# Optimization experiments

Hardware: AMD Instinct MI355X
Metric: run time of the kernel (lower is better)

Reference implementation:

```python
import jax, jax.numpy as jnp
import numpy as np

B, N, F_DIM, C_DIM, L = 4, 2048, 64, 64, 3

def setup_inputs() -> dict:
    key = jax.random.key(0)
    k1, k2, k3 = jax.random.split(key, 3)
    V = jax.random.normal(k1, (B, N, F_DIM), dtype=jnp.float32)
    A = jax.random.uniform(k2, (B, N, N, L), dtype=jnp.float32)
    h_weights = jax.random.normal(k3, (L + 1, C_DIM, F_DIM), dtype=jnp.float32) * 0.05
    return {"V": V, "A": A, "h_weights": h_weights}

def reference(V, A, h_weights):
    # Original math: A_aug = concat([I, A], -1)  (identity as edge-type 0)
    # H[b,i,j,c,f] = sum_l A_aug[b,i,j,l] * h_weights[l,c,f]
    # V_out[b,i,c] = sum_{j,f} H[b,i,j,c,f] * V[b,j,f]; relu.
    # The identity edge-type contributes h_weights[0] @ V[b,i] directly,
    # avoiding materializing the concatenated (B,N,N,L+1) tensor.
    self_term = jnp.einsum('cf,bif->bic', h_weights[0], V)        # (B,N,C)
    rel_term = jnp.einsum('bijl,lcf,bjf->bic', A, h_weights[1:], V)
    return jax.nn.relu(self_term + rel_term)
```

## Files before the change

kernel.cpp:

```cpp
#include <hip/hip_runtime.h>
#include <cstdint>

#define BDIM 4
#define NDIM 2048
#define FDIM 64
#define CDIM 64
#define LDIM 3
#define KTOT (NDIM * LDIM)
#define BK 256
#define NSTEP (KTOT / BK)
#define KB (KTOT / 32)

typedef __attribute__((ext_vector_type(4))) float f32x4;
typedef __attribute__((ext_vector_type(8))) short s16x8;
typedef __attribute__((ext_vector_type(4))) unsigned int u32x4;

__device__ __forceinline__ unsigned short f2bf(float x) {
  union { float f; uint32_t u; } v; v.f = x;
  uint32_t r = v.u + 0x7FFFu + ((v.u >> 16) & 1u);
  return (unsigned short)(r >> 16);
}

__device__ __forceinline__ uint32_t cvtpk(float lo, float hi) {
  uint32_t r;
  asm("v_cvt_pk_bf16_f32 %0, %1, %2" : "=v"(r) : "v"(lo), "v"(hi));
  return r;
}

__global__ __launch_bounds__(64) void k1_precompute(
    const float* __restrict__ V, const float* __restrict__ hw,
    float* __restrict__ S, unsigned short* __restrict__ Ut3) {
  const int j0 = blockIdx.x * 16;
  const int le = blockIdx.y;
  const int b  = blockIdx.z;
  const int lane = threadIdx.x;
  const int q = lane & 15, g = lane >> 4;

  const float* vrow = V + ((size_t)(b * NDIM + j0 + q)) * FDIM + g * 8;
  f32x4 va0 = *(const f32x4*)(vrow);
  f32x4 va1 = *(const f32x4*)(vrow + 4);
  f32x4 va2 = *(const f32x4*)(vrow + 32);
  f32x4 va3 = *(const f32x4*)(vrow + 36);
  s16x8 a0, a1;
#pragma unroll
  for (int e = 0; e < 4; ++e) {
    a0[e]     = (short)f2bf(va0[e]);
    a0[e + 4] = (short)f2bf(va1[e]);
    a1[e]     = (short)f2bf(va2[e]);
    a1[e + 4] = (short)f2bf(va3[e]);
  }

  const float* hbase = hw + (size_t)le * CDIM * FDIM;
#pragma unroll
  for (int ct = 0; ct < 4; ++ct) {
    const float* hrow = hbase + (size_t)(ct * 16 + q) * FDIM + g * 8;
    f32x4 hb0 = *(const f32x4*)(hrow);
    f32x4 hb1 = *(const f32x4*)(hrow + 4);
    f32x4 hb2 = *(const f32x4*)(hrow + 32);
    f32x4 hb3 = *(const f32x4*)(hrow + 36);
    s16x8 b0, b1;
#pragma unroll
    for (int e = 0; e < 4; ++e) {
      b0[e]     = (short)f2bf(hb0[e]);
      b0[e + 4] = (short)f2bf(hb1[e]);
      b1[e]     = (short)f2bf(hb2[e]);
      b1[e + 4] = (short)f2bf(hb3[e]);
    }
    f32x4 acc = {0.f, 0.f, 0.f, 0.f};
    acc = __builtin_amdgcn_mfma_f32_16x16x32_bf16(a0, b0, acc, 0, 0, 0);
    acc = __builtin_amdgcn_mfma_f32_16x16x32_bf16(a1, b1, acc, 0, 0, 0);
    if (le == 0) {
#pragma unroll
      for (int rr = 0; rr < 4; ++rr) {
        int j = j0 + g * 4 + rr;
        S[((size_t)b * NDIM + j) * CDIM + ct * 16 + q] = acc[rr];
      }
    } else {
#pragma unroll
      for (int rr = 0; rr < 4; ++rr) {
        int j = j0 + g * 4 + rr;
        int k = j * 3 + (le - 1);
        int kb = k >> 5, gg = (k >> 3) & 3, ee = k & 7;
        size_t off = ((size_t)b * KB + kb) * 2048 + (size_t)ct * 512 +
                     (size_t)gg * 128 + (size_t)q * 8 + ee;
        Ut3[off] = f2bf(acc[rr]);
      }
    }
  }
}

__global__ __launch_bounds__(256) void k2_main(
    const float* __restrict__ A, const unsigned short* __restrict__ Ut3,
    const float* __restrict__ S, float* __restrict__ out) {
  __shared__ float Abuf[4][4096];

  const int bid = blockIdx.x;
  const int swz = (bid & 7) * 64 + (bid >> 3);
  const int b   = swz >> 7;
  const int i0  = (swz & 127) * 16;
  const int tid = threadIdx.x;
  const int lane = tid & 63, w = tid >> 6;
  const int q = lane & 15, g = lane >> 4, q7 = q & 7;

  const int r0 = 4 * w;
  const float* ag0 = A + ((size_t)(b * NDIM + i0 + r0 + 0)) * KTOT + ((lane ^ ((r0 + 0) & 7)) * 4);
  const float* ag1 = A + ((size_t)(b * NDIM + i0 + r0 + 1)) * KTOT + ((lane ^ ((r0 + 1) & 7)) * 4);
  const float* ag2 = A + ((size_t)(b * NDIM + i0 + r0 + 2)) * KTOT + ((lane ^ ((r0 + 2) & 7)) * 4);
  const float* ag3 = A + ((size_t)(b * NDIM + i0 + r0 + 3)) * KTOT + ((lane ^ ((r0 + 3) & 7)) * 4);

  const unsigned short* bgp = Ut3 + (size_t)b * KB * 2048 + w * 512 + lane * 8;

  float* ldsw = &Abuf[0][0] + r0 * 256 + lane * 4;

#define GLL4(slot)                                                            \
  do {                                                                        \
    __builtin_amdgcn_global_load_lds(                                         \
        (__attribute__((address_space(1))) void*)(ag0),                       \
        (__attribute__((address_space(3))) void*)(ldsw + (slot) * 4096), 16, 0, 0); \
    __builtin_amdgcn_global_load_lds(                                         \
        (__attribute__((address_space(1))) void*)(ag1),                       \
        (__attribute__((address_space(3))) void*)(ldsw + (slot) * 4096 + 256), 16, 0, 0); \
    __builtin_amdgcn_global_load_lds(                                         \
        (__attribute__((address_space(1))) void*)(ag2),                       \
        (__attribute__((address_space(3))) void*)(ldsw + (slot) * 4096 + 512), 16, 0, 0); \
    __builtin_amdgcn_global_load_lds(                                         \
        (__attribute__((address_space(1))) void*)(ag3),                       \
        (__attribute__((address_space(3))) void*)(ldsw + (slot) * 4096 + 768), 16, 0, 0); \
  } while (0)

#define LDB(BW)                                                               \
  do {                                                                        \
    _Pragma("unroll")                                                         \
    for (int t = 0; t < 8; ++t)                                               \
      BW[t] = *(const s16x8*)(bgp + (size_t)t * 2048);                        \
  } while (0)

  f32x4 accA = {0.f, 0.f, 0.f, 0.f}, accB = {0.f, 0.f, 0.f, 0.f};
  s16x8 bA[8], bB[8];

  GLL4(0); ag0 += BK; ag1 += BK; ag2 += BK; ag3 += BK;
  GLL4(1); ag0 += BK; ag1 += BK; ag2 += BK; ag3 += BK;
  LDB(bA); bgp += 8 * 2048;

  int s = 0;
#define K2STEP(BW, BR)                                                        \
  do {                                                                        \
    GLL4((s + 2) & 3);                                                        \
    if (s + 2 < NSTEP - 1) { ag0 += BK; ag1 += BK; ag2 += BK; ag3 += BK; }    \
    LDB(BW);                                                                  \
    if (s + 2 < NSTEP) bgp += 8 * 2048;                                       \
    asm volatile("s_waitcnt vmcnt(12)" ::: "memory");                         \
    __builtin_amdgcn_sched_barrier(0);                                        \
    __builtin_amdgcn_s_barrier();                                             \
    __builtin_amdgcn_sched_barrier(0);                                        \
    const float* rowp = &Abuf[s & 3][0] + q * 256;                            \
    _Pragma("unroll")                                                         \
    for (int kk = 0; kk < 8; ++kk) {                                          \
      f32x4 a0 = *(const f32x4*)(rowp + ((kk * 8 + ((2 * g) ^ q7)) << 2));    \
      f32x4 a1 = *(const f32x4*)(rowp + ((kk * 8 + ((2 * g + 1) ^ q7)) << 2));\
      u32x4 wv;                                                               \
      wv[0] = cvtpk(a0[0], a0[1]); wv[1] = cvtpk(a0[2], a0[3]);               \
      wv[2] = cvtpk(a1[0], a1[1]); wv[3] = cvtpk(a1[2], a1[3]);               \
      if (kk & 1)                                                             \
        accB = __builtin_amdgcn_mfma_f32_16x16x32_bf16(                       \
            __builtin_bit_cast(s16x8, wv), BR[kk], accB, 0, 0, 0);            \
      else                                                                    \
        accA = __builtin_amdgcn_mfma_f32_16x16x32_bf16(                       \
            __builtin_bit_cast(s16x8, wv), BR[kk], accA, 0, 0, 0);            \
    }                                                                         \
    ++s;                                                                      \
  } while (0)

  for (int it = 0; it < NSTEP / 2; ++it) {
    K2STEP(bB, bA);
    K2STEP(bA, bB);
  }
#undef K2STEP
#undef GLL4
#undef LDB

  asm volatile("s_waitcnt vmcnt(0)" ::: "memory");

  f32x4 acc = accA + accB;
  const int c = w * 16 + q;
#pragma unroll
  for (int rr = 0; rr < 4; ++rr) {
    int i = i0 + g * 4 + rr;
    size_t idx = ((size_t)(b * NDIM) + i) * CDIM + c;
    float v = acc[rr] + S[idx];
    out[idx] = v > 0.f ? v : 0.f;
  }
}

extern "C" void kernel_launch(void* const* d_in, const int* in_sizes, int n_in,
                              void* d_out, int out_size, void* d_ws, size_t ws_size,
                              hipStream_t stream) {
  const float* V  = (const float*)d_in[0];
  const float* A  = (const float*)d_in[1];
  const float* hw = (const float*)d_in[2];
  float* out = (float*)d_out;

  float* S = (float*)d_ws;
  unsigned short* Ut3 =
      (unsigned short*)((char*)d_ws + (size_t)BDIM * NDIM * CDIM * sizeof(float));

  k1_precompute<<<dim3(NDIM / 16, LDIM + 1, BDIM), 64, 0, stream>>>(V, hw, S, Ut3);
  k2_main<<<dim3((NDIM / 16) * BDIM), 256, 0, stream>>>(A, Ut3, S, out);
}
```

Before: 47.97 us.

## Retile main GEMM to 32-row blocks with 2x2 warp layout and BK=128

Changes the main kernel tile from 16 rows x 64 channels per block to 32 rows x 64 channels, with four warps arranged 2x2 so that each warp computes 16 rows by 32 channels using two accumulators. The K step per stage is halved to 128 so the LDS buffer size stays the same. This halves the grid and halves how often the Ut3 B operand is re-read from global memory across row blocks. The trade-off is fewer blocks (256) for the GPU's CUs to share, more pipeline steps, and a changed wait-count schedule.

```diff
diff --git a/kernel.cpp b/kernel.cpp
--- a/kernel.cpp
+++ b/kernel.cpp
@@ -7,7 +7,7 @@
 #define CDIM 64
 #define LDIM 3
 #define KTOT (NDIM * LDIM)
-#define BK 256
+#define BK 128
 #define NSTEP (KTOT / BK)
 #define KB (KTOT / 32)
 
@@ -95,78 +95,88 @@
   __shared__ float Abuf[4][4096];
 
   const int bid = blockIdx.x;
-  const int swz = (bid & 7) * 64 + (bid >> 3);
-  const int b   = swz >> 7;
-  const int i0  = (swz & 127) * 16;
+  const int swz = (bid & 7) * 32 + (bid >> 3);
+  const int b   = swz >> 6;
+  const int i0  = (swz & 63) * 32;
   const int tid = threadIdx.x;
   const int lane = tid & 63, w = tid >> 6;
   const int q = lane & 15, g = lane >> 4, q7 = q & 7;
-
-  const int r0 = 4 * w;
-  const float* ag0 = A + ((size_t)(b * NDIM + i0 + r0 + 0)) * KTOT + ((lane ^ ((r0 + 0) & 7)) * 4);
-  const float* ag1 = A + ((size_t)(b * NDIM + i0 + r0 + 1)) * KTOT + ((lane ^ ((r0 + 1) & 7)) * 4);
-  const float* ag2 = A + ((size_t)(b * NDIM + i0 + r0 + 2)) * KTOT + ((lane ^ ((r0 + 2) & 7)) * 4);
-  const float* ag3 = A + ((size_t)(b * NDIM + i0 + r0 + 3)) * KTOT + ((lane ^ ((r0 + 3) & 7)) * 4);
-
-  const unsigned short* bgp = Ut3 + (size_t)b * KB * 2048 + w * 512 + lane * 8;
-
-  float* ldsw = &Abuf[0][0] + r0 * 256 + lane * 4;
+  const int wr = w >> 1, wc = w & 1;
+
+  const int arowA = 8 * w + ((lane >> 5) & 1);
+  const float* agp[4];
+#pragma unroll
+  for (int t = 0; t < 4; ++t) {
+    int r = 8 * w + 2 * t + (lane >> 5);
+    int gran = (lane & 31) ^ (r & 7);
+    agp[t] = A + ((size_t)(b * NDIM + i0 + r)) * KTOT + gran * 4;
+  }
+  (void)arowA;
+
+  const unsigned short* bgp =
+      Ut3 + (size_t)b * KB * 2048 + (size_t)(wc * 2) * 512 + (size_t)lane * 8;
+
+  float* ldsw = &Abuf[0][0] + w * 1024 + lane * 4;
 
 #define GLL4(slot)                                                            \
   do {                                                                        \
     __builtin_amdgcn_global_load_lds(                                         \
-        (__attribute__((address_space(1))) void*)(ag0),                       \
+        (__attribute__((address_space(1))) void*)(agp[0]),                    \
         (__attribute__((address_space(3))) void*)(ldsw + (slot) * 4096), 16, 0, 0); \
     __builtin_amdgcn_global_load_lds(                                         \
-        (__attribute__((address_space(1))) void*)(ag1),                       \
+        (__attribute__((address_space(1))) void*)(agp[1]),                    \
         (__attribute__((address_space(3))) void*)(ldsw + (slot) * 4096 + 256), 16, 0, 0); \
     __builtin_amdgcn_global_load_lds(                                         \
-        (__attribute__((address_space(1))) void*)(ag2),                       \
+        (__attribute__((address_space(1))) void*)(agp[2]),                    \
         (__attribute__((address_space(3))) void*)(ldsw + (slot) * 4096 + 512), 16, 0, 0); \
     __builtin_amdgcn_global_load_lds(                                         \
-        (__attribute__((address_space(1))) void*)(ag3),                       \
+        (__attribute__((address_space(1))) void*)(agp[3]),                    \
         (__attribute__((address_space(3))) void*)(ldsw + (slot) * 4096 + 768), 16, 0, 0); \
   } while (0)
+
+#define AADV(cond)                                                            \
+  do { if (cond) { agp[0] += BK; agp[1] += BK; agp[2] += BK; agp[3] += BK; } } while (0)
 
 #define LDB(BW)                                                               \
   do {                                                                        \
     _Pragma("unroll")                                                         \
-    for (int t = 0; t < 8; ++t)                                               \
-      BW[t] = *(const s16x8*)(bgp + (size_t)t * 2048);                        \
+    for (int t = 0; t < 4; ++t) {                                             \
+      BW[t * 2 + 0] = *(const s16x8*)(bgp + (size_t)t * 2048);                \
+      BW[t * 2 + 1] = *(const s16x8*)(bgp + (size_t)t * 2048 + 512);          \
+    }                                                                         \
   } while (0)
 
-  f32x4 accA = {0.f, 0.f, 0.f, 0.f}, accB = {0.f, 0.f, 0.f, 0.f};
+  f32x4 acc0 = {0.f, 0.f, 0.f, 0.f}, acc1 = {0.f, 0.f, 0.f, 0.f};
   s16x8 bA[8], bB[8];
 
-  GLL4(0); ag0 += BK; ag1 += BK; ag2 += BK; ag3 += BK;
-  GLL4(1); ag0 += BK; ag1 += BK; ag2 += BK; ag3 += BK;
-  LDB(bA); bgp += 8 * 2048;
+  GLL4(0); AADV(true);
+  LDB(bA); bgp += 4 * 2048;
+  GLL4(1); AADV(true);
 
   int s = 0;
 #define K2STEP(BW, BR)                                                        \
   do {                                                                        \
+    LDB(BW);                                                                  \
+    if (s + 2 < NSTEP) bgp += 4 * 2048;       \
+    __builtin_amdgcn_sched_barrier(0);                                        \
     GLL4((s + 2) & 3);                                                        \
-    if (s + 2 < NSTEP - 1) { ag0 += BK; ag1 += BK; ag2 += BK; ag3 += BK; }    \
-    LDB(BW);                                                                  \
-    if (s + 2 < NSTEP) bgp += 8 * 2048;                                       \
-    asm volatile("s_waitcnt vmcnt(12)" ::: "memory");                         \
+    AADV(s + 3 < NSTEP);   \
+    asm volatile("s_waitcnt vmcnt(16)" ::: "memory");                         \
     __builtin_amdgcn_sched_barrier(0);                                        \
     __builtin_amdgcn_s_barrier();                                             \
     __builtin_amdgcn_sched_barrier(0);                                        \
-    const float* rowp = &Abuf[s & 3][0] + q * 256;                            \
+    const float* rowp = &Abuf[s & 3][0] + (wr * 16 + q) * 128;                \
     _Pragma("unroll")                                                         \
-    for (int kk = 0; kk < 8; ++kk) {                                          \
+    for (int kk = 0; kk < 4; ++kk) {                                          \
       f32x4 a0 = *(const f32x4*)(rowp + ((kk * 8 + ((2 * g) ^ q7)) << 2));    \
       f32x4 a1 = *(const f32x4*)(rowp + ((kk * 8 + ((2 * g + 1) ^ q7)) << 2));\
       u32x4 wv;                                                               \
       wv[0] = cvtpk(a0[0], a0[1]); wv[1] = cvtpk(a0[2], a0[3]);               \
       wv[2] = cvtpk(a1[0], a1[1]); wv[3] = cvtpk(a1[2], a1[3]);               \
-      if (kk & 1)                                                             \
-        accB = __builtin_amdgcn_mfma_f32_16x16x32_bf16(                       \
-            __builtin_bit_cast(s16x8, wv), BR[kk], accB, 0, 0, 0);            \
-      else                                                                    \
-        accA = __builtin_amdgcn_mfma_f32_16x16x32_bf16(                       \
-            __builtin_bit_cast(s16x8, wv), BR[kk], accA, 0, 0, 0);            \
+      acc0 = __builtin_amdgcn_mfma_f32_16x16x32_bf16(                         \
+          __builtin_bit_cast(s16x8, wv), BR[kk * 2 + 0], acc0, 0, 0, 0);      \
+      acc1 = __builtin_amdgcn_mfma_f32_16x16x32_bf16(                         \
+          __builtin_bit_cast(s16x8, wv), BR[kk * 2 + 1], acc1, 0, 0, 0);      \
     }                                                                         \
     ++s;                                                                      \
   } while (0)
@@ -177,18 +187,22 @@
   }
 #undef K2STEP
 #undef GLL4
+#undef AADV
 #undef LDB
 
   asm volatile("s_waitcnt vmcnt(0)" ::: "memory");
 
-  f32x4 acc = accA + accB;
-  const int c = w * 16 + q;
-#pragma unroll
-  for (int rr = 0; rr < 4; ++rr) {
-    int i = i0 + g * 4 + rr;
-    size_t idx = ((size_t)(b * NDIM) + i) * CDIM + c;
-    float v = acc[rr] + S[idx];
-    out[idx] = v > 0.f ? v : 0.f;
+  const int c = wc * 32 + q;
+#pragma unroll
+  for (int ct = 0; ct < 2; ++ct) {
+    f32x4 av = ct ? acc1 : acc0;
+#pragma unroll
+    for (int rr = 0; rr < 4; ++rr) {
+      int i = i0 + wr * 16 + g * 4 + rr;
+      size_t idx = ((size_t)(b * NDIM) + i) * CDIM + c + ct * 16;
+      float v = av[rr] + S[idx];
+      out[idx] = v > 0.f ? v : 0.f;
+    }
   }
 }
 
@@ -205,5 +219,5 @@
       (unsigned short*)((char*)d_ws + (size_t)BDIM * NDIM * CDIM * sizeof(float));
 
   k1_precompute<<<dim3(NDIM / 16, LDIM + 1, BDIM), 64, 0, stream>>>(V, hw, S, Ut3);
-  k2_main<<<dim3((NDIM / 16) * BDIM), 256, 0, stream>>>(A, Ut3, S, out);
-}
+  k2_main<<<dim3((NDIM / 32) * BDIM), 256, 0, stream>>>(A, Ut3, S, out);
+}
```

Result: slower. 53.76 us (+12.1%).

## Switch A staging to double-buffered 512-wide K tiles with split-half compute

Applied to the files above, without the earlier changes.

The main kernel moves from a four-slot ring of 256-wide K tiles to a two-slot double buffer of 512-wide tiles, keeping the same shared-memory footprint. Each step is now computed in two halves, with the B-operand loads for the second half interleaved between them. The goal is fewer barriers and pipeline steps per K, each carrying more work. In exchange, prefetch depth drops, an extra barrier is added per step, and the in-order vmcnt wait before the second half also forces the next A tile's loads to finish early. That last effect can serialize memory behind compute.

```diff
diff --git a/kernel.cpp b/kernel.cpp
--- a/kernel.cpp
+++ b/kernel.cpp
@@ -7,7 +7,7 @@
 #define CDIM 64
 #define LDIM 3
 #define KTOT (NDIM * LDIM)
-#define BK 256
+#define BK 512
 #define NSTEP (KTOT / BK)
 #define KB (KTOT / 32)
 
@@ -92,7 +92,7 @@
 __global__ __launch_bounds__(256) void k2_main(
     const float* __restrict__ A, const unsigned short* __restrict__ Ut3,
     const float* __restrict__ S, float* __restrict__ out) {
-  __shared__ float Abuf[4][4096];
+  __shared__ float Abuf[2][8192];
 
   const int bid = blockIdx.x;
   const int swz = (bid & 7) * 64 + (bid >> 3);
@@ -102,62 +102,57 @@
   const int lane = tid & 63, w = tid >> 6;
   const int q = lane & 15, g = lane >> 4, q7 = q & 7;
 
-  const int r0 = 4 * w;
-  const float* ag0 = A + ((size_t)(b * NDIM + i0 + r0 + 0)) * KTOT + ((lane ^ ((r0 + 0) & 7)) * 4);
-  const float* ag1 = A + ((size_t)(b * NDIM + i0 + r0 + 1)) * KTOT + ((lane ^ ((r0 + 1) & 7)) * 4);
-  const float* ag2 = A + ((size_t)(b * NDIM + i0 + r0 + 2)) * KTOT + ((lane ^ ((r0 + 2) & 7)) * 4);
-  const float* ag3 = A + ((size_t)(b * NDIM + i0 + r0 + 3)) * KTOT + ((lane ^ ((r0 + 3) & 7)) * 4);
-
-  const unsigned short* bgp = Ut3 + (size_t)b * KB * 2048 + w * 512 + lane * 8;
-
-  float* ldsw = &Abuf[0][0] + r0 * 256 + lane * 4;
-
-#define GLL4(slot)                                                            \
+  const float* agp[4];
+#pragma unroll
+  for (int t = 0; t < 4; ++t) {
+    int r = 4 * w + t;
+    agp[t] = A + ((size_t)(b * NDIM + i0 + r)) * KTOT + ((lane ^ (r & 7)) * 4);
+  }
+
+  const unsigned short* bgp =
+      Ut3 + (size_t)b * KB * 2048 + (size_t)w * 512 + (size_t)lane * 8;
+
+  float* ldsw = &Abuf[0][0] + w * 4 * 512 + lane * 4;
+
+#define GLL8(slot)                                                            \
   do {                                                                        \
-    __builtin_amdgcn_global_load_lds(                                         \
-        (__attribute__((address_space(1))) void*)(ag0),                       \
-        (__attribute__((address_space(3))) void*)(ldsw + (slot) * 4096), 16, 0, 0); \
-    __builtin_amdgcn_global_load_lds(                                         \
-        (__attribute__((address_space(1))) void*)(ag1),                       \
-        (__attribute__((address_space(3))) void*)(ldsw + (slot) * 4096 + 256), 16, 0, 0); \
-    __builtin_amdgcn_global_load_lds(                                         \
-        (__attribute__((address_space(1))) void*)(ag2),                       \
-        (__attribute__((address_space(3))) void*)(ldsw + (slot) * 4096 + 512), 16, 0, 0); \
-    __builtin_amdgcn_global_load_lds(                                         \
-        (__attribute__((address_space(1))) void*)(ag3),                       \
-        (__attribute__((address_space(3))) void*)(ldsw + (slot) * 4096 + 768), 16, 0, 0); \
+    _Pragma("unroll")                                                         \
+    for (int t = 0; t < 4; ++t) {                                             \
+      __builtin_amdgcn_global_load_lds(                                       \
+          (__attribute__((address_space(1))) void*)(agp[t]),                  \
+          (__attribute__((address_space(3))) void*)(ldsw + (slot) * 8192 + t * 512), \
+          16, 0, 0);                                                          \
+      __builtin_amdgcn_global_load_lds(                                       \
+          (__attribute__((address_space(1))) void*)(agp[t] + 256),            \
+          (__attribute__((address_space(3))) void*)(ldsw + (slot) * 8192 + t * 512 + 256), \
+          16, 0, 0);                                                          \
+    }                                                                         \
   } while (0)
 
-#define LDB(BW)                                                               \
+#define AADV(cond)                                                            \
+  do { if (cond) { agp[0] += BK; agp[1] += BK; agp[2] += BK; agp[3] += BK; } } while (0)
+
+#define LDB(BW, kbase)                                                        \
   do {                                                                        \
     _Pragma("unroll")                                                         \
     for (int t = 0; t < 8; ++t)                                               \
-      BW[t] = *(const s16x8*)(bgp + (size_t)t * 2048);                        \
+      BW[t] = *(const s16x8*)(bgp + (size_t)((kbase) + t) * 2048);            \
   } while (0)
 
   f32x4 accA = {0.f, 0.f, 0.f, 0.f}, accB = {0.f, 0.f, 0.f, 0.f};
   s16x8 bA[8], bB[8];
 
-  GLL4(0); ag0 += BK; ag1 += BK; ag2 += BK; ag3 += BK;
-  GLL4(1); ag0 += BK; ag1 += BK; ag2 += BK; ag3 += BK;
-  LDB(bA); bgp += 8 * 2048;
-
-  int s = 0;
-#define K2STEP(BW, BR)                                                        \
+  GLL8(0); AADV(true);
+  LDB(bA, 0);
+
+#define HALF(half, BR)                                                        \
   do {                                                                        \
-    GLL4((s + 2) & 3);                                                        \
-    if (s + 2 < NSTEP - 1) { ag0 += BK; ag1 += BK; ag2 += BK; ag3 += BK; }    \
-    LDB(BW);                                                                  \
-    if (s + 2 < NSTEP) bgp += 8 * 2048;                                       \
-    asm volatile("s_waitcnt vmcnt(12)" ::: "memory");                         \
-    __builtin_amdgcn_sched_barrier(0);                                        \
-    __builtin_amdgcn_s_barrier();                                             \
-    __builtin_amdgcn_sched_barrier(0);                                        \
-    const float* rowp = &Abuf[s & 3][0] + q * 256;                            \
+    const float* rowp = &Abuf[s & 1][0] + q * 512;                            \
     _Pragma("unroll")                                                         \
     for (int kk = 0; kk < 8; ++kk) {                                          \
-      f32x4 a0 = *(const f32x4*)(rowp + ((kk * 8 + ((2 * g) ^ q7)) << 2));    \
-      f32x4 a1 = *(const f32x4*)(rowp + ((kk * 8 + ((2 * g + 1) ^ q7)) << 2));\
+      int kg = (half) * 8 + kk;                                               \
+      f32x4 a0 = *(const f32x4*)(rowp + ((kg * 8 + ((2 * g) ^ q7)) << 2));    \
+      f32x4 a1 = *(const f32x4*)(rowp + ((kg * 8 + ((2 * g + 1) ^ q7)) << 2));\
       u32x4 wv;                                                               \
       wv[0] = cvtpk(a0[0], a0[1]); wv[1] = cvtpk(a0[2], a0[3]);               \
       wv[2] = cvtpk(a1[0], a1[1]); wv[3] = cvtpk(a1[2], a1[3]);               \
@@ -168,15 +163,27 @@
         accA = __builtin_amdgcn_mfma_f32_16x16x32_bf16(                       \
             __builtin_bit_cast(s16x8, wv), BR[kk], accA, 0, 0, 0);            \
     }                                                                         \
-    ++s;                                                                      \
   } while (0)
 
-  for (int it = 0; it < NSTEP / 2; ++it) {
-    K2STEP(bB, bA);
-    K2STEP(bA, bB);
-  }
-#undef K2STEP
-#undef GLL4
+  for (int s = 0; s < NSTEP; ++s) {
+    GLL8((s + 1) & 1);
+    AADV(s + 2 < NSTEP);
+    LDB(bB, 8);
+    if (s + 1 < NSTEP) bgp += 16 * 2048;
+    asm volatile("s_waitcnt vmcnt(16)" ::: "memory");
+    __builtin_amdgcn_sched_barrier(0);
+    __builtin_amdgcn_s_barrier();
+    __builtin_amdgcn_sched_barrier(0);
+    HALF(0, bA);
+    LDB(bA, 0);
+    asm volatile("s_waitcnt vmcnt(8)" ::: "memory");
+    __builtin_amdgcn_sched_barrier(0);
+    HALF(1, bB);
+    __builtin_amdgcn_s_barrier();
+  }
+#undef HALF
+#undef GLL8
+#undef AADV
 #undef LDB
 
   asm volatile("s_waitcnt vmcnt(0)" ::: "memory");
```

Result: slower. 49.55 us (+3.3%).
